# Performance work log

Measured on AMD Instinct MI355X. Metric: run time of the kernel, lower is better.

## Reference

```python
import jax, jax.numpy as jnp
import numpy as np

B, S, D = 2, 2048, 1024
H = 16
HD = D // H  # head dim 64


def setup_inputs() -> dict:
    key = jax.random.key(0)
    ks = jax.random.split(key, 7)
    queries = jax.random.normal(ks[0], (B, S, D), dtype=jnp.float32)
    keys = jax.random.normal(ks[1], (B, S, D), dtype=jnp.float32)
    values = jax.random.normal(ks[2], (B, S, D), dtype=jnp.float32)
    scale = 1.0 / np.sqrt(D)
    Wq = jax.random.normal(ks[3], (D, D), dtype=jnp.float32) * scale
    Wk = jax.random.normal(ks[4], (D, D), dtype=jnp.float32) * scale
    Wv = jax.random.normal(ks[5], (D, D), dtype=jnp.float32) * scale
    Wo = jax.random.normal(ks[6], (D, D), dtype=jnp.float32) * scale
    return {"queries": queries, "keys": keys, "values": values,
            "Wq": Wq, "Wk": Wk, "Wv": Wv, "Wo": Wo}


def _split_heads(x):
    # [B,S,D] -> [B,H,S,HD]
    b, s, d = x.shape
    return x.reshape(b, s, H, d // H).transpose(0, 2, 1, 3)


def reference(queries, keys, values, Wq, Wk, Wv, Wo):
    q = _split_heads(queries @ Wq) * (HD ** -0.5)   # [B,H,S,HD]
    k = _split_heads(keys @ Wk)
    v = _split_heads(values @ Wv)
    logits = jnp.einsum('bhqd,bhkd->bhqk', q, k)     # [B,H,S,S]
    weights = jax.nn.softmax(logits, axis=-1)
    ctx = jnp.einsum('bhqk,bhkd->bhqd', weights, v)  # [B,H,S,HD]
    ctx = ctx.transpose(0, 2, 1, 3).reshape(B, S, D)
    return ctx @ Wo
```

## Files before the change

### kernel.cpp

```cpp
#include <hip/hip_runtime.h>
#include <hip/hip_bf16.h>


typedef short s16x8 __attribute__((ext_vector_type(8)));
typedef float f32x4v __attribute__((ext_vector_type(4)));
typedef float f32x16v __attribute__((ext_vector_type(16)));
typedef unsigned int u32x4v __attribute__((ext_vector_type(4)));

__device__ inline unsigned short f2bf(float f) {
    union { float f; unsigned int i; } x; x.f = f;
    unsigned int r = x.i + 0x7FFFu + ((x.i >> 16) & 1u);
    return (unsigned short)(r >> 16);
}
__device__ inline unsigned int pkbf(float lo, float hi) {
    return (unsigned int)f2bf(lo) | ((unsigned int)f2bf(hi) << 16);
}

__device__ inline void gld_lds16(const unsigned short* g, unsigned short* l) {
    __builtin_amdgcn_global_load_lds(
        (const __attribute__((address_space(1))) unsigned int*)(const void*)g,
        (__attribute__((address_space(3))) unsigned int*)(void*)l,
        16, 0, 0);
}

__global__ __launch_bounds__(256)
void cvt3(const float* __restrict__ W0, const float* __restrict__ W1, const float* __restrict__ W2,
          unsigned short* __restrict__ T0, unsigned short* __restrict__ T1, unsigned short* __restrict__ T2) {
    const float* W = (blockIdx.z == 0) ? W0 : (blockIdx.z == 1) ? W1 : W2;
    unsigned short* Wt = (blockIdx.z == 0) ? T0 : (blockIdx.z == 1) ? T1 : T2;
    __shared__ __align__(16) unsigned short Ls[64 * 72];
    const int t = threadIdx.x;
    const int k0 = blockIdx.y * 64, n0 = blockIdx.x * 64;
    const int r = t >> 4, c4 = (t & 15) * 4;
    #pragma unroll
    for (int i = 0; i < 4; ++i) {
        float4 wv = *(const float4*)&W[(size_t)(k0 + r + i * 16) * 1024 + n0 + c4];
        Ls[(c4 + 0) * 72 + r + i * 16] = f2bf(wv.x);
        Ls[(c4 + 1) * 72 + r + i * 16] = f2bf(wv.y);
        Ls[(c4 + 2) * 72 + r + i * 16] = f2bf(wv.z);
        Ls[(c4 + 3) * 72 + r + i * 16] = f2bf(wv.w);
    }
    __syncthreads();
    #pragma unroll
    for (int i = 0; i < 2; ++i) {
        const int p = i * 256 + t;
        const int n = p & 63, kc = p >> 6;
        s16x8 v = *(const s16x8*)&Ls[n * 72 + kc * 8];
        const int gn = n0 + n, k = k0 + kc * 8;
        const size_t g = ((size_t)(gn >> 7) * 128 + (k >> 3)) * 128 + (gn & 127);
        *(s16x8*)&Wt[g * 8] = v;
    }
}

__global__ __launch_bounds__(256, 3)
void gemm_qkv(const float* __restrict__ A0, const float* __restrict__ A1, const float* __restrict__ A2,
              const unsigned short* __restrict__ W0, const unsigned short* __restrict__ W1,
              const unsigned short* __restrict__ W2,
              unsigned short* __restrict__ OQ, unsigned short* __restrict__ OK,
              unsigned short* __restrict__ OV, float scaleQ) {
    const int z = blockIdx.z;
    const float* Av = (z == 0) ? A0 : (z == 1) ? A1 : A2;
    const unsigned short* Bsw = (z == 0) ? W0 : (z == 1) ? W1 : W2;
    const float scale = (z == 0) ? scaleQ : 1.0f;

    __shared__ __align__(16) unsigned short Al[1024 * 8];
    __shared__ __align__(16) unsigned short Bl[1024 * 8];
    const int t = threadIdx.x;
    const int lane = t & 63, w = t >> 6;
    const int ln = lane & 15, qd = lane >> 4;
    const int mw = (w & 1) * 64, nw = (w >> 1) * 64;
    const int m0 = blockIdx.y * 128, n0 = blockIdx.x * 128;

    f32x4v acc[4][4] = {};

    for (int k0 = 0; k0 < 1024; k0 += 64) {
        __syncthreads();
        {
            const size_t gb = ((size_t)(n0 >> 7) * 128 + (k0 >> 3)) * 128;
            #pragma unroll
            for (int j = 0; j < 4; ++j)
                gld_lds16(Bsw + (gb + j * 256 + t) * 8, &Bl[(j * 256 + w * 64) * 8]);
        }
        #pragma unroll
        for (int j = 0; j < 4; ++j) {
            const int p = j * 256 + t;
            const int row = p >> 3, kc = p & 7;
            const float* src = Av + (size_t)(m0 + row) * 1024 + k0 + kc * 8;
            float4 f0 = ((const float4*)src)[0];
            float4 f1 = ((const float4*)src)[1];
            uint4 u;
            u.x = pkbf(f0.x, f0.y); u.y = pkbf(f0.z, f0.w);
            u.z = pkbf(f1.x, f1.y); u.w = pkbf(f1.z, f1.w);
            *(uint4*)&Al[(kc * 128 + (row ^ kc)) * 8] = u;
        }
        __syncthreads();

        #pragma unroll
        for (int kk = 0; kk < 2; ++kk) {
            const int kc = kk * 4 + qd;
            s16x8 a[4], b[4];
            #pragma unroll
            for (int mt = 0; mt < 4; ++mt)
                a[mt] = *(const s16x8*)&Al[(kc * 128 + ((mw + mt * 16 + ln) ^ kc)) * 8];
            #pragma unroll
            for (int nt = 0; nt < 4; ++nt)
                b[nt] = *(const s16x8*)&Bl[(kc * 128 + nw + nt * 16 + ln) * 8];
            #pragma unroll
            for (int mt = 0; mt < 4; ++mt)
                #pragma unroll
                for (int nt = 0; nt < 4; ++nt)
                    acc[mt][nt] = __builtin_amdgcn_mfma_f32_16x16x32_bf16(a[mt], b[nt], acc[mt][nt], 0, 0, 0);
        }
    }

    #pragma unroll
    for (int mt = 0; mt < 4; ++mt)
        #pragma unroll
        for (int nt = 0; nt < 4; ++nt)
            #pragma unroll
            for (int i = 0; i < 4; ++i) {
                const int m = m0 + mw + mt * 16 + qd * 4 + i;
                const int n = n0 + nw + nt * 16 + ln;
                const float v = acc[mt][nt][i] * scale;
                const int bh = (m >> 11) * 16 + (n >> 6), s = m & 2047, hd = n & 63;
                if (z == 0) {
                    OQ[((size_t)bh * 2048 + s) * 64 + hd] = f2bf(v);
                } else if (z == 1) {
                    const size_t g = ((size_t)(bh * 32 + (s >> 6)) * 8 + (hd >> 3)) * 64 + (s & 63);
                    OK[g * 8 + (hd & 7)] = f2bf(v);
                } else {
                    const size_t g = ((size_t)(bh * 32 + (s >> 6)) * 8 + ((s >> 3) & 7)) * 64 + hd;
                    OV[g * 8 + (s & 7)] = f2bf(v);
                }
            }
}

__global__ __launch_bounds__(256, 2)
void gemm_out(const unsigned short* __restrict__ Asw, const unsigned short* __restrict__ Bsw,
              float* __restrict__ outF) {
    __shared__ __align__(16) unsigned short Al[1024 * 8];
    __shared__ __align__(16) unsigned short Bl[512 * 8];
    const int t = threadIdx.x;
    const int lane = t & 63, w = t >> 6;
    const int ln = lane & 15, qd = lane >> 4;
    const int mw = (w & 1) * 64, nw = (w >> 1) * 32;
    const int m0 = blockIdx.y * 128, n0 = blockIdx.x * 64;

    f32x4v acc[4][2] = {};

    for (int k0 = 0; k0 < 1024; k0 += 64) {
        __syncthreads();
        {
            const size_t ga = ((size_t)(m0 >> 7) * 128 + (k0 >> 3)) * 128;
            #pragma unroll
            for (int j = 0; j < 4; ++j)
                gld_lds16(Asw + (ga + j * 256 + t) * 8, &Al[(j * 256 + w * 64) * 8]);
        }
        {
            #pragma unroll
            for (int i = 0; i < 2; ++i) {
                const int c = w * 2 + i;
                const size_t gb = ((size_t)(n0 >> 7) * 128 + (k0 >> 3) + c) * 128 + (n0 & 127) + lane;
                gld_lds16(Bsw + gb * 8, &Bl[(c * 64) * 8]);
            }
        }
        __syncthreads();

        #pragma unroll
        for (int kk = 0; kk < 2; ++kk) {
            const int kc = kk * 4 + qd;
            s16x8 a[4], b[2];
            #pragma unroll
            for (int mt = 0; mt < 4; ++mt)
                a[mt] = *(const s16x8*)&Al[(kc * 128 + mw + mt * 16 + ln) * 8];
            #pragma unroll
            for (int nt = 0; nt < 2; ++nt)
                b[nt] = *(const s16x8*)&Bl[(kc * 64 + nw + nt * 16 + ln) * 8];
            #pragma unroll
            for (int mt = 0; mt < 4; ++mt)
                #pragma unroll
                for (int nt = 0; nt < 2; ++nt)
                    acc[mt][nt] = __builtin_amdgcn_mfma_f32_16x16x32_bf16(a[mt], b[nt], acc[mt][nt], 0, 0, 0);
        }
    }

    #pragma unroll
    for (int mt = 0; mt < 4; ++mt)
        #pragma unroll
        for (int nt = 0; nt < 2; ++nt)
            #pragma unroll
            for (int i = 0; i < 4; ++i) {
                const int m = m0 + mw + mt * 16 + qd * 4 + i;
                const int n = n0 + nw + nt * 16 + ln;
                outF[(size_t)m * 1024 + n] = acc[mt][nt][i];
            }
}


__device__ __forceinline__ void fa_compute(
        const unsigned short* Ksb, const unsigned short* Vsb,
        const int H, const int l31, const s16x8* qf,
        f32x16v* accO, float& ls0, float& ls1, float& ls2, float& ls3) {
    f32x16v accS[2] = {};
    #pragma unroll
    for (int kk = 0; kk < 4; ++kk) {
        s16x8 kf0 = *(const s16x8*)&Ksb[((kk * 2 + H) * 64 + l31) * 8];
        s16x8 kf1 = *(const s16x8*)&Ksb[((kk * 2 + H) * 64 + 32 + l31) * 8];
        accS[0] = __builtin_amdgcn_mfma_f32_32x32x16_bf16(kf0, qf[kk], accS[0], 0, 0, 0);
        accS[1] = __builtin_amdgcn_mfma_f32_32x32x16_bf16(kf1, qf[kk], accS[1], 0, 0, 0);
    }

    u32x4v af[4];
    #pragma unroll
    for (int mt = 0; mt < 2; ++mt) {
        float p[16];
        #pragma unroll
        for (int r = 0; r < 16; ++r)
            p[r] = exp2f(accS[mt][r]);
        #pragma unroll
        for (int r = 0; r < 16; r += 4) {
            ls0 += p[r + 0]; ls1 += p[r + 1]; ls2 += p[r + 2]; ls3 += p[r + 3];
        }
        unsigned int C[8];
        #pragma unroll
        for (int j = 0; j < 8; ++j)
            asm("v_cvt_pk_bf16_f32 %0, %1, %2" : "=v"(C[j]) : "v"(p[2 * j]), "v"(p[2 * j + 1]));
        #pragma unroll
        for (int pp = 0; pp < 2; ++pp) {
            unsigned int x0 = C[4 * pp + 0], y0 = C[4 * pp + 2];
            unsigned int x1 = C[4 * pp + 1], y1 = C[4 * pp + 3];
            asm("v_permlane32_swap_b32 %0, %1" : "+v"(x0), "+v"(y0));
            asm("v_permlane32_swap_b32 %0, %1" : "+v"(x1), "+v"(y1));
            u32x4v a; a.x = x0; a.y = x1; a.z = y0; a.w = y1;
            af[mt * 2 + pp] = a;
        }
    }

    #pragma unroll
    for (int kk2 = 0; kk2 < 4; ++kk2) {
        s16x8 a = __builtin_bit_cast(s16x8, af[kk2]);
        s16x8 vf0 = *(const s16x8*)&Vsb[((kk2 * 2 + H) * 64 + l31) * 8];
        s16x8 vf1 = *(const s16x8*)&Vsb[((kk2 * 2 + H) * 64 + 32 + l31) * 8];
        accO[0] = __builtin_amdgcn_mfma_f32_32x32x16_bf16(a, vf0, accO[0], 0, 0, 0);
        accO[1] = __builtin_amdgcn_mfma_f32_32x32x16_bf16(a, vf1, accO[1], 0, 0, 0);
    }
}

__global__ __launch_bounds__(256, 2)
void fattn(const unsigned short* __restrict__ Q, const unsigned short* __restrict__ Ksw,
           const unsigned short* __restrict__ Vsw, unsigned short* __restrict__ ctx) {
    __shared__ __align__(16) unsigned short Ks3[3][512 * 8];
    __shared__ __align__(16) unsigned short Vs3[3][512 * 8];

    const int t = threadIdx.x, lane = t & 63, w = t >> 6;
    const int l31 = lane & 31, H = lane >> 5;
    const int bid = blockIdx.x + (blockIdx.y << 4);
    const int wid = (bid & 7) * 64 + (bid >> 3);
    const int bh = wid >> 4, m0 = (wid & 15) * 128;
    const size_t head = (size_t)bh * 2048 * 64;

    s16x8 qf[4];
    #pragma unroll
    for (int kk = 0; kk < 4; ++kk)
        qf[kk] = *(const s16x8*)(Q + head + (size_t)(m0 + w * 32 + l31) * 64 + kk * 16 + H * 8);
    asm volatile("s_waitcnt vmcnt(0)" ::: "memory");
    #pragma unroll
    for (int kk = 0; kk < 4; ++kk) {
        u32x4v q = __builtin_bit_cast(u32x4v, qf[kk]);
        asm volatile("" : "+v"(q.x), "+v"(q.y), "+v"(q.z), "+v"(q.w));
        qf[kk] = __builtin_bit_cast(s16x8, q);
    }

    const size_t tb = (size_t)bh * 32 * 512;
    {
        #pragma unroll
        for (int kt = 0; kt < 2; ++kt)
            #pragma unroll
            for (int j = 0; j < 2; ++j) {
                gld_lds16(Ksw + (tb + kt * 512 + j * 256 + t) * 8, &Ks3[kt][(j * 256 + w * 64) * 8]);
                gld_lds16(Vsw + (tb + kt * 512 + j * 256 + t) * 8, &Vs3[kt][(j * 256 + w * 64) * 8]);
            }
    }

    f32x16v accO[2] = {};
    float ls0 = 0.f, ls1 = 0.f, ls2 = 0.f, ls3 = 0.f;

    int cur = 0;
    for (int kt = 0; kt < 31; ++kt) {
        asm volatile("s_waitcnt vmcnt(4)" ::: "memory");
        __builtin_amdgcn_s_barrier();
        asm volatile("" ::: "memory");
        if (kt < 30) {
            const int ib = (cur == 0) ? 2 : cur - 1;
            const size_t tbn = tb + (size_t)(kt + 2) * 512;
            #pragma unroll
            for (int j = 0; j < 2; ++j) {
                gld_lds16(Ksw + (tbn + j * 256 + t) * 8, &Ks3[ib][(j * 256 + w * 64) * 8]);
                gld_lds16(Vsw + (tbn + j * 256 + t) * 8, &Vs3[ib][(j * 256 + w * 64) * 8]);
            }
        }
        fa_compute(Ks3[cur], Vs3[cur], H, l31, qf, accO, ls0, ls1, ls2, ls3);
        cur = (cur == 2) ? 0 : cur + 1;
    }
    asm volatile("s_waitcnt vmcnt(0)" ::: "memory");
    __builtin_amdgcn_s_barrier();
    asm volatile("" ::: "memory");
    fa_compute(Ks3[cur], Vs3[cur], H, l31, qf, accO, ls0, ls1, ls2, ls3);

    float lsum = (ls0 + ls1) + (ls2 + ls3);
    lsum += __shfl_xor(lsum, 32, 64);
    const float inv = 1.f / lsum;

    #pragma unroll
    for (int r = 0; r < 16; ++r) {
        const int qloc = (r & 3) + 8 * (r >> 2) + 4 * H;
        const float rinv = __shfl(inv, qloc, 64);
        const int mrow = (bh >> 4) * 2048 + m0 + w * 32 + qloc;
        #pragma unroll
        for (int nt = 0; nt < 2; ++nt) {
            const int k = (bh & 15) * 64 + nt * 32 + l31;
            const size_t g = ((size_t)(mrow >> 7) * 128 + (k >> 3)) * 128 + (mrow & 127);
            ctx[g * 8 + (k & 7)] = f2bf(accO[nt][r] * rinv);
        }
    }
}

extern "C" void kernel_launch(void* const* d_in, const int* in_sizes, int n_in,
                              void* d_out, int out_size, void* d_ws, size_t ws_size,
                              hipStream_t stream) {
    char* ws = (char*)d_ws;
    unsigned short* Qb  = (unsigned short*)(ws);
    unsigned short* Ksw = (unsigned short*)(ws + ((size_t)8 << 20));
    unsigned short* Vsw = (unsigned short*)(ws + ((size_t)16 << 20));
    unsigned short* Wqt = (unsigned short*)(ws + ((size_t)24 << 20));
    unsigned short* Wkt = (unsigned short*)(ws + ((size_t)26 << 20));
    unsigned short* Wvt = (unsigned short*)(ws + ((size_t)28 << 20));
    unsigned short* ctx = (unsigned short*)(ws + ((size_t)24 << 20));
    unsigned short* Wot = (unsigned short*)(ws);

    cvt3<<<dim3(16, 16, 3), 256, 0, stream>>>((const float*)d_in[3], (const float*)d_in[4],
                                              (const float*)d_in[5], Wqt, Wkt, Wvt);

    gemm_qkv<<<dim3(8, 32, 3), 256, 0, stream>>>(
        (const float*)d_in[0], (const float*)d_in[1], (const float*)d_in[2],
        Wqt, Wkt, Wvt, Qb, Ksw, Vsw, 0.125f * 1.44269504f);

    fattn<<<dim3(16, 32), dim3(256), 0, stream>>>(Qb, Ksw, Vsw, ctx);

    cvt3<<<dim3(16, 16, 1), 256, 0, stream>>>((const float*)d_in[6], nullptr, nullptr,
                                              Wot, nullptr, nullptr);

    gemm_out<<<dim3(16, 32), 256, 0, stream>>>(ctx, Wot, (float*)d_out);
}
```

Baseline: 241.3 us.

## Pre-pack activations to bf16 and double-buffer async GEMM loads with tile remap

Adds a separate cvtA kernel that converts the fp32 Q/K/V inputs into a swizzled bf16 tile layout. The QKV projection GEMM can then stream both operands with direct global-to-LDS loads, double-buffered with a 32-wide k step and explicit vmcnt waits. The output GEMM gets the same two-stage pipeline, and both GEMMs use a 1D grid with remapped block indices, likely for cache/XCD locality. This costs an extra conversion kernel and extra workspace traffic, and the path only runs when the workspace is at least 54 MB; otherwise it falls back to the old fused-convert kernel.

```diff
diff --git a/kernel.cpp b/kernel.cpp
--- a/kernel.cpp
+++ b/kernel.cpp
@@ -52,64 +52,101 @@
     }
 }
 
+__global__ __launch_bounds__(256)
+void cvtA(const float* __restrict__ A0, const float* __restrict__ A1, const float* __restrict__ A2,
+          unsigned short* __restrict__ O0, unsigned short* __restrict__ O1, unsigned short* __restrict__ O2) {
+    const float* A = (blockIdx.z == 0) ? A0 : (blockIdx.z == 1) ? A1 : A2;
+    unsigned short* O = (blockIdx.z == 0) ? O0 : (blockIdx.z == 1) ? O1 : O2;
+    __shared__ __align__(16) unsigned short Ls[8192];
+    const int t = threadIdx.x;
+    const int k0 = blockIdx.x * 64, rp = blockIdx.y;
+    const int row = t >> 1, kh = (t & 1) * 32;
+    const float* src = A + (size_t)(rp * 128 + row) * 1024 + k0 + kh;
+    float4 f[8];
+    #pragma unroll
+    for (int i = 0; i < 8; ++i) f[i] = ((const float4*)src)[i];
+    #pragma unroll
+    for (int j = 0; j < 4; ++j) {
+        uint4 u;
+        u.x = pkbf(f[j * 2].x, f[j * 2].y);
+        u.y = pkbf(f[j * 2].z, f[j * 2].w);
+        u.z = pkbf(f[j * 2 + 1].x, f[j * 2 + 1].y);
+        u.w = pkbf(f[j * 2 + 1].z, f[j * 2 + 1].w);
+        const int kc = (t & 1) * 4 + j;
+        *(uint4*)&Ls[(kc * 128 + row) * 8] = u;
+    }
+    __syncthreads();
+    const size_t gbase = ((size_t)rp * 128 + (k0 >> 3)) * 128;
+    #pragma unroll
+    for (int i = 0; i < 4; ++i) {
+        const int idx = i * 256 + t;
+        *(uint4*)&O[(gbase + idx) * 8] = *(const uint4*)&Ls[idx * 8];
+    }
+}
+
 __global__ __launch_bounds__(256, 3)
-void gemm_qkv(const float* __restrict__ A0, const float* __restrict__ A1, const float* __restrict__ A2,
+void gemm_qkv(const unsigned short* __restrict__ Aq, const unsigned short* __restrict__ Ak,
+              const unsigned short* __restrict__ Av,
               const unsigned short* __restrict__ W0, const unsigned short* __restrict__ W1,
               const unsigned short* __restrict__ W2,
               unsigned short* __restrict__ OQ, unsigned short* __restrict__ OK,
               unsigned short* __restrict__ OV, float scaleQ) {
-    const int z = blockIdx.z;
-    const float* Av = (z == 0) ? A0 : (z == 1) ? A1 : A2;
+    const int p = blockIdx.x;
+    const int L = (p & 7) * 96 + (p >> 3);
+    const int z = L >> 8;
+    const int rem = L & 255;
+    const int m0 = (rem >> 3) * 128, n0 = (rem & 7) * 128;
+    const unsigned short* Asw = (z == 0) ? Aq : (z == 1) ? Ak : Av;
     const unsigned short* Bsw = (z == 0) ? W0 : (z == 1) ? W1 : W2;
     const float scale = (z == 0) ? scaleQ : 1.0f;
 
-    __shared__ __align__(16) unsigned short Al[1024 * 8];
-    __shared__ __align__(16) unsigned short Bl[1024 * 8];
-    const int t = threadIdx.x;
-    const int lane = t & 63, w = t >> 6;
+    __shared__ __align__(16) unsigned short Al[2][4096];
+    __shared__ __align__(16) unsigned short Bl[2][4096];
+    const int t = threadIdx.x, lane = t & 63, w = t >> 6;
     const int ln = lane & 15, qd = lane >> 4;
     const int mw = (w & 1) * 64, nw = (w >> 1) * 64;
-    const int m0 = blockIdx.y * 128, n0 = blockIdx.x * 128;
+    const size_t gaB = (size_t)(m0 >> 7) * 16384;
+    const size_t gbB = (size_t)(n0 >> 7) * 16384;
 
     f32x4v acc[4][4] = {};
 
-    for (int k0 = 0; k0 < 1024; k0 += 64) {
-        __syncthreads();
+    auto stage = [&](int kt, int b) {
+        const size_t ga = gaB + (size_t)kt * 512;
+        const size_t gb = gbB + (size_t)kt * 512;
+        #pragma unroll
+        for (int j = 0; j < 2; ++j)
+            gld_lds16(Asw + (ga + j * 256 + t) * 8, &Al[b][(j * 256 + w * 64) * 8]);
+        #pragma unroll
+        for (int j = 0; j < 2; ++j)
+            gld_lds16(Bsw + (gb + j * 256 + t) * 8, &Bl[b][(j * 256 + w * 64) * 8]);
+    };
+
+    stage(0, 0);
+    stage(1, 1);
+    for (int kt = 0; kt < 32; ++kt) {
+        if (kt < 31) asm volatile("s_waitcnt vmcnt(4)" ::: "memory");
+        else         asm volatile("s_waitcnt vmcnt(0)" ::: "memory");
+        __builtin_amdgcn_s_barrier();
+        asm volatile("" ::: "memory");
+        const int b = kt & 1;
         {
-            const size_t gb = ((size_t)(n0 >> 7) * 128 + (k0 >> 3)) * 128;
-            #pragma unroll
-            for (int j = 0; j < 4; ++j)
-                gld_lds16(Bsw + (gb + j * 256 + t) * 8, &Bl[(j * 256 + w * 64) * 8]);
-        }
-        #pragma unroll
-        for (int j = 0; j < 4; ++j) {
-            const int p = j * 256 + t;
-            const int row = p >> 3, kc = p & 7;
-            const float* src = Av + (size_t)(m0 + row) * 1024 + k0 + kc * 8;
-            float4 f0 = ((const float4*)src)[0];
-            float4 f1 = ((const float4*)src)[1];
-            uint4 u;
-            u.x = pkbf(f0.x, f0.y); u.y = pkbf(f0.z, f0.w);
-            u.z = pkbf(f1.x, f1.y); u.w = pkbf(f1.z, f1.w);
-            *(uint4*)&Al[(kc * 128 + (row ^ kc)) * 8] = u;
-        }
-        __syncthreads();
-
-        #pragma unroll
-        for (int kk = 0; kk < 2; ++kk) {
-            const int kc = kk * 4 + qd;
-            s16x8 a[4], b[4];
-            #pragma unroll
-            for (int mt = 0; mt < 4; ++mt)
-                a[mt] = *(const s16x8*)&Al[(kc * 128 + ((mw + mt * 16 + ln) ^ kc)) * 8];
+            s16x8 a[4], bb[4];
+            #pragma unroll
+            for (int mt = 0; mt < 4; ++mt)
+                a[mt] = *(const s16x8*)&Al[b][(qd * 128 + mw + mt * 16 + ln) * 8];
             #pragma unroll
             for (int nt = 0; nt < 4; ++nt)
-                b[nt] = *(const s16x8*)&Bl[(kc * 128 + nw + nt * 16 + ln) * 8];
+                bb[nt] = *(const s16x8*)&Bl[b][(qd * 128 + nw + nt * 16 + ln) * 8];
             #pragma unroll
             for (int mt = 0; mt < 4; ++mt)
                 #pragma unroll
                 for (int nt = 0; nt < 4; ++nt)
-                    acc[mt][nt] = __builtin_amdgcn_mfma_f32_16x16x32_bf16(a[mt], b[nt], acc[mt][nt], 0, 0, 0);
+                    acc[mt][nt] = __builtin_amdgcn_mfma_f32_16x16x32_bf16(a[mt], bb[nt], acc[mt][nt], 0, 0, 0);
+        }
+        if (kt < 30) {
+            __builtin_amdgcn_s_barrier();
+            asm volatile("" ::: "memory");
+            stage(kt + 2, b);
         }
     }
 
@@ -135,52 +172,147 @@
             }
 }
 
+__global__ __launch_bounds__(256, 3)
+void gemm_qkv_pack(const float* __restrict__ A0, const float* __restrict__ A1, const float* __restrict__ A2,
+                   const unsigned short* __restrict__ W0, const unsigned short* __restrict__ W1,
+                   const unsigned short* __restrict__ W2,
+                   unsigned short* __restrict__ OQ, unsigned short* __restrict__ OK,
+                   unsigned short* __restrict__ OV, float scaleQ) {
+    const int z = blockIdx.z;
+    const float* Avv = (z == 0) ? A0 : (z == 1) ? A1 : A2;
+    const unsigned short* Bsw = (z == 0) ? W0 : (z == 1) ? W1 : W2;
+    const float scale = (z == 0) ? scaleQ : 1.0f;
+
+    __shared__ __align__(16) unsigned short Al[1024 * 8];
+    __shared__ __align__(16) unsigned short Bl[1024 * 8];
+    const int t = threadIdx.x;
+    const int lane = t & 63, w = t >> 6;
+    const int ln = lane & 15, qd = lane >> 4;
+    const int mw = (w & 1) * 64, nw = (w >> 1) * 64;
+    const int m0 = blockIdx.y * 128, n0 = blockIdx.x * 128;
+
+    f32x4v acc[4][4] = {};
+
+    for (int k0 = 0; k0 < 1024; k0 += 64) {
+        __syncthreads();
+        {
+            const size_t gb = ((size_t)(n0 >> 7) * 128 + (k0 >> 3)) * 128;
+            #pragma unroll
+            for (int j = 0; j < 4; ++j)
+                gld_lds16(Bsw + (gb + j * 256 + t) * 8, &Bl[(j * 256 + w * 64) * 8]);
+        }
+        #pragma unroll
+        for (int j = 0; j < 4; ++j) {
+            const int pp = j * 256 + t;
+            const int row = pp >> 3, kc = pp & 7;
+            const float* src = Avv + (size_t)(m0 + row) * 1024 + k0 + kc * 8;
+            float4 f0 = ((const float4*)src)[0];
+            float4 f1 = ((const float4*)src)[1];
+            uint4 u;
+            u.x = pkbf(f0.x, f0.y); u.y = pkbf(f0.z, f0.w);
+            u.z = pkbf(f1.x, f1.y); u.w = pkbf(f1.z, f1.w);
+            *(uint4*)&Al[(kc * 128 + (row ^ kc)) * 8] = u;
+        }
+        __syncthreads();
+
+        #pragma unroll
+        for (int kk = 0; kk < 2; ++kk) {
+            const int kc = kk * 4 + qd;
+            s16x8 a[4], b[4];
+            #pragma unroll
+            for (int mt = 0; mt < 4; ++mt)
+                a[mt] = *(const s16x8*)&Al[(kc * 128 + ((mw + mt * 16 + ln) ^ kc)) * 8];
+            #pragma unroll
+            for (int nt = 0; nt < 4; ++nt)
+                b[nt] = *(const s16x8*)&Bl[(kc * 128 + nw + nt * 16 + ln) * 8];
+            #pragma unroll
+            for (int mt = 0; mt < 4; ++mt)
+                #pragma unroll
+                for (int nt = 0; nt < 4; ++nt)
+                    acc[mt][nt] = __builtin_amdgcn_mfma_f32_16x16x32_bf16(a[mt], b[nt], acc[mt][nt], 0, 0, 0);
+        }
+    }
+
+    #pragma unroll
+    for (int mt = 0; mt < 4; ++mt)
+        #pragma unroll
+        for (int nt = 0; nt < 4; ++nt)
+            #pragma unroll
+            for (int i = 0; i < 4; ++i) {
+                const int m = m0 + mw + mt * 16 + qd * 4 + i;
+                const int n = n0 + nw + nt * 16 + ln;
+                const float v = acc[mt][nt][i] * scale;
+                const int bh = (m >> 11) * 16 + (n >> 6), s = m & 2047, hd = n & 63;
+                if (z == 0) {
+                    OQ[((size_t)bh * 2048 + s) * 64 + hd] = f2bf(v);
+                } else if (z == 1) {
+                    const size_t g = ((size_t)(bh * 32 + (s >> 6)) * 8 + (hd >> 3)) * 64 + (s & 63);
+                    OK[g * 8 + (hd & 7)] = f2bf(v);
+                } else {
+                    const size_t g = ((size_t)(bh * 32 + (s >> 6)) * 8 + ((s >> 3) & 7)) * 64 + hd;
+                    OV[g * 8 + (s & 7)] = f2bf(v);
+                }
+            }
+}
+
 __global__ __launch_bounds__(256, 2)
 void gemm_out(const unsigned short* __restrict__ Asw, const unsigned short* __restrict__ Bsw,
               float* __restrict__ outF) {
-    __shared__ __align__(16) unsigned short Al[1024 * 8];
-    __shared__ __align__(16) unsigned short Bl[512 * 8];
-    const int t = threadIdx.x;
-    const int lane = t & 63, w = t >> 6;
+    const int p = blockIdx.x;
+    const int L = (p & 7) * 64 + (p >> 3);
+    const int m0 = (L >> 4) * 128, n0 = (L & 15) * 64;
+
+    __shared__ __align__(16) unsigned short Al[2][8192];
+    __shared__ __align__(16) unsigned short Bl[2][4096];
+    const int t = threadIdx.x, lane = t & 63, w = t >> 6;
     const int ln = lane & 15, qd = lane >> 4;
     const int mw = (w & 1) * 64, nw = (w >> 1) * 32;
-    const int m0 = blockIdx.y * 128, n0 = blockIdx.x * 64;
+    const size_t gaB = (size_t)(m0 >> 7) * 16384;
+    const size_t gbB = (size_t)(n0 >> 7) * 16384 + (n0 & 127);
 
     f32x4v acc[4][2] = {};
 
-    for (int k0 = 0; k0 < 1024; k0 += 64) {
-        __syncthreads();
-        {
-            const size_t ga = ((size_t)(m0 >> 7) * 128 + (k0 >> 3)) * 128;
-            #pragma unroll
-            for (int j = 0; j < 4; ++j)
-                gld_lds16(Asw + (ga + j * 256 + t) * 8, &Al[(j * 256 + w * 64) * 8]);
-        }
-        {
-            #pragma unroll
-            for (int i = 0; i < 2; ++i) {
-                const int c = w * 2 + i;
-                const size_t gb = ((size_t)(n0 >> 7) * 128 + (k0 >> 3) + c) * 128 + (n0 & 127) + lane;
-                gld_lds16(Bsw + gb * 8, &Bl[(c * 64) * 8]);
-            }
-        }
-        __syncthreads();
-
+    auto stage = [&](int kt, int b) {
+        const size_t ga = gaB + (size_t)kt * 1024;
+        #pragma unroll
+        for (int j = 0; j < 4; ++j)
+            gld_lds16(Asw + (ga + j * 256 + t) * 8, &Al[b][(j * 256 + w * 64) * 8]);
+        #pragma unroll
+        for (int i = 0; i < 2; ++i) {
+            const int c = w * 2 + i;
+            const size_t gb = gbB + (size_t)(kt * 8 + c) * 128 + lane;
+            gld_lds16(Bsw + gb * 8, &Bl[b][(c * 64) * 8]);
+        }
+    };
+
+    stage(0, 0);
+    stage(1, 1);
+    for (int kt = 0; kt < 16; ++kt) {
+        if (kt < 15) asm volatile("s_waitcnt vmcnt(6)" ::: "memory");
+        else         asm volatile("s_waitcnt vmcnt(0)" ::: "memory");
+        __builtin_amdgcn_s_barrier();
+        asm volatile("" ::: "memory");
+        const int b = kt & 1;
         #pragma unroll
         for (int kk = 0; kk < 2; ++kk) {
             const int kc = kk * 4 + qd;
-            s16x8 a[4], b[2];
-            #pragma unroll
-            for (int mt = 0; mt < 4; ++mt)
-                a[mt] = *(const s16x8*)&Al[(kc * 128 + mw + mt * 16 + ln) * 8];
+            s16x8 a[4], bb[2];
+            #pragma unroll
+            for (int mt = 0; mt < 4; ++mt)
+                a[mt] = *(const s16x8*)&Al[b][(kc * 128 + mw + mt * 16 + ln) * 8];
             #pragma unroll
             for (int nt = 0; nt < 2; ++nt)
-                b[nt] = *(const s16x8*)&Bl[(kc * 64 + nw + nt * 16 + ln) * 8];
+                bb[nt] = *(const s16x8*)&Bl[b][(kc * 64 + nw + nt * 16 + ln) * 8];
             #pragma unroll
             for (int mt = 0; mt < 4; ++mt)
                 #pragma unroll
                 for (int nt = 0; nt < 2; ++nt)
-                    acc[mt][nt] = __builtin_amdgcn_mfma_f32_16x16x32_bf16(a[mt], b[nt], acc[mt][nt], 0, 0, 0);
+                    acc[mt][nt] = __builtin_amdgcn_mfma_f32_16x16x32_bf16(a[mt], bb[nt], acc[mt][nt], 0, 0, 0);
+        }
+        if (kt < 14) {
+            __builtin_amdgcn_s_barrier();
+            asm volatile("" ::: "memory");
+            stage(kt + 2, b);
         }
     }
 
@@ -195,7 +327,6 @@
                 outF[(size_t)m * 1024 + n] = acc[mt][nt][i];
             }
 }
-
 
 __device__ __forceinline__ void fa_compute(
         const unsigned short* Ksb, const unsigned short* Vsb,
@@ -335,20 +466,32 @@
     unsigned short* Wqt = (unsigned short*)(ws + ((size_t)24 << 20));
     unsigned short* Wkt = (unsigned short*)(ws + ((size_t)26 << 20));
     unsigned short* Wvt = (unsigned short*)(ws + ((size_t)28 << 20));
+    unsigned short* Aq  = (unsigned short*)(ws + ((size_t)30 << 20));
+    unsigned short* Ak  = (unsigned short*)(ws + ((size_t)38 << 20));
+    unsigned short* Av  = (unsigned short*)(ws + ((size_t)46 << 20));
     unsigned short* ctx = (unsigned short*)(ws + ((size_t)24 << 20));
     unsigned short* Wot = (unsigned short*)(ws);
 
+    const bool big = ws_size >= ((size_t)54 << 20);
+
     cvt3<<<dim3(16, 16, 3), 256, 0, stream>>>((const float*)d_in[3], (const float*)d_in[4],
                                               (const float*)d_in[5], Wqt, Wkt, Wvt);
 
-    gemm_qkv<<<dim3(8, 32, 3), 256, 0, stream>>>(
-        (const float*)d_in[0], (const float*)d_in[1], (const float*)d_in[2],
-        Wqt, Wkt, Wvt, Qb, Ksw, Vsw, 0.125f * 1.44269504f);
+    if (big) {
+        cvtA<<<dim3(16, 32, 3), 256, 0, stream>>>((const float*)d_in[0], (const float*)d_in[1],
+                                                  (const float*)d_in[2], Aq, Ak, Av);
+        gemm_qkv<<<dim3(768), 256, 0, stream>>>(Aq, Ak, Av, Wqt, Wkt, Wvt,
+                                                Qb, Ksw, Vsw, 0.125f * 1.44269504f);
+    } else {
+        gemm_qkv_pack<<<dim3(8, 32, 3), 256, 0, stream>>>(
+            (const float*)d_in[0], (const float*)d_in[1], (const float*)d_in[2],
+            Wqt, Wkt, Wvt, Qb, Ksw, Vsw, 0.125f * 1.44269504f);
+    }
 
     fattn<<<dim3(16, 32), dim3(256), 0, stream>>>(Qb, Ksw, Vsw, ctx);
 
     cvt3<<<dim3(16, 16, 1), 256, 0, stream>>>((const float*)d_in[6], nullptr, nullptr,
                                               Wot, nullptr, nullptr);
 
-    gemm_out<<<dim3(16, 32), 256, 0, stream>>>(ctx, Wot, (float*)d_out);
-}
+    gemm_out<<<dim3(512), 256, 0, stream>>>(ctx, Wot, (float*)d_out);
+}
```

Result: faster. 233.0 us (-3.4%).
